# Kernel optimization log

Hardware: AMD Instinct MI355X
Metric: run time of the kernel (lower is better)

Reference implementation:

```python
import jax, jax.numpy as jnp
import numpy as np

N = 100000          # nodes
E = 6400000         # edges (avg degree 64)
V0 = 1.0            # self.v0 (source assigns v0 despite u0 arg)
W0 = 1.0            # self.w0
EPS = 1e-12         # torch F.normalize eps


def setup_inputs() -> dict:
    key = jax.random.key(0)
    k1, k2, k3, k4 = jax.random.split(key, 4)
    return {
        "x": jax.random.normal(k1, (N, 1), dtype=jnp.float32),
        "theta": jax.random.normal(k2, (N, 1), dtype=jnp.float32),
        "edge_src": jax.random.randint(k3, (E,), 0, N, dtype=jnp.int64),
        "edge_dst": jax.random.randint(k4, (E,), 0, N, dtype=jnp.int64),
    }


def reference(x, theta, edge_src, edge_dst):
    # node velocity: v = v0 * [cos(theta), sin(theta)]  -> [N, 2]
    v = V0 * jnp.concatenate([jnp.cos(theta), jnp.sin(theta)], axis=-1)

    # per-edge message: dtheta = x[src] - theta[dst]; m = [cos, sin]  -> [E, 2]
    dtheta = x[edge_src] - theta[edge_dst]            # [E, 1]
    msg = jnp.concatenate([jnp.cos(dtheta), jnp.sin(dtheta)], axis=-1)  # [E, 2]

    # mailbox mean over incoming edges per dst node (segment mean)
    seg_sum = jax.ops.segment_sum(msg, edge_dst, num_segments=N)               # [N, 2]
    cnt = jax.ops.segment_sum(jnp.ones((E, 1), msg.dtype), edge_dst, num_segments=N)
    mean_cs = seg_sum / jnp.maximum(cnt, 1.0)

    # torque: w = w0 * normalize(mean_cs)[..., 1:2]  (L2-normalize, torch eps)
    norm = jnp.maximum(jnp.linalg.norm(mean_cs, axis=-1, keepdims=True), EPS)
    w = W0 * (mean_cs / norm)[..., 1:2]               # [N, 1]

    # updated ndata packed as [v_x, v_y, w]
    return jnp.concatenate([v, w], axis=-1)           # [N, 3]
```

## Files before the change

kernel.cpp:

```cpp
#include <hip/hip_runtime.h>
#include <math.h>


#define EPS 1e-12f
#define NPART 16
#define RNODES 6250
#define RMAX 6250
#define BLK 1024

#define NBIN 512
#define BINBLK 512
#define CAP 1024
#define OCAP 262144

static __device__ __forceinline__ unsigned long long pack_cs(float xv) {
    float sn, cs;
    __sincosf(xv, &sn, &cs);
    const int ci = __float2int_rn(cs * 32768.0f);
    const int si = __float2int_rn(sn * 32768.0f);
    return (1ull << 52)
         | ((unsigned long long)(unsigned)(si + 32768) << 26)
         | (unsigned long long)(unsigned)(ci + 32768);
}

__global__ __launch_bounds__(256) void prep_pack_kernel(
        const float* __restrict__ x,
        unsigned long long* __restrict__ pu,
        int* __restrict__ oflow_cnt, int N) {
    int i = blockIdx.x * blockDim.x + threadIdx.x;
    if (i < N) pu[i] = pack_cs(x[i]);
    else if (i == N && oflow_cnt) pu[N] = 0ull;
    if (i == 0 && oflow_cnt) *oflow_cnt = 0;
}

__global__ __launch_bounds__(BINBLK) void bin_kernel(
        const int* __restrict__ esrc,
        const int* __restrict__ edst,
        unsigned* __restrict__ records,
        int* __restrict__ counts,
        unsigned long long* __restrict__ oflow,
        int* __restrict__ oflow_cnt,
        int E, int N) {
    __shared__ int lcur[NPART];
    if (threadIdx.x < NPART) lcur[threadIdx.x] = 0;
    __syncthreads();

    const int chunk = (((E + NBIN - 1) / NBIN) + 3) & ~3;
    const int beg = blockIdx.x * chunk;
    const int end = min(beg + chunk, E);
    const int end4 = beg + (max(end - beg, 0) & ~3);
    unsigned* __restrict__ myrec =
        records + (size_t)blockIdx.x * (NPART * CAP);

    for (int i = beg + threadIdx.x * 4; i < end4; i += BINBLK * 4) {
        const int4 d4 = *(const int4*)&edst[i];
        const int4 s4 = *(const int4*)&esrc[i];
        const int dv[4] = {d4.x, d4.y, d4.z, d4.w};
        const int sv[4] = {s4.x, s4.y, s4.z, s4.w};
        #pragma unroll
        for (int j = 0; j < 4; ++j) {
            const unsigned d = (unsigned)dv[j];
            const unsigned p = d / RNODES;
            const unsigned dl = d - p * RNODES;
            const unsigned rec = ((unsigned)sv[j] << 13) | dl;
            const int slot = atomicAdd(&lcur[p], 1);
            if (slot < CAP) {
                myrec[p * CAP + slot] = rec;
            } else {
                const int g = atomicAdd(oflow_cnt, 1);
                if (g < OCAP)
                    oflow[g] = ((unsigned long long)(unsigned)sv[j] << 32) | d;
            }
        }
    }
    for (int i = end4 + threadIdx.x; i < end; i += BINBLK) {
        const unsigned d = (unsigned)edst[i];
        const unsigned p = d / RNODES;
        const unsigned dl = d - p * RNODES;
        const unsigned rec = ((unsigned)esrc[i] << 13) | dl;
        const int slot = atomicAdd(&lcur[p], 1);
        if (slot < CAP) {
            myrec[p * CAP + slot] = rec;
        } else {
            const int g = atomicAdd(oflow_cnt, 1);
            if (g < OCAP)
                oflow[g] = ((unsigned long long)(unsigned)esrc[i] << 32) | d;
        }
    }

    __syncthreads();
    if (threadIdx.x < NPART) {
        const int c = min(lcur[threadIdx.x], CAP);
        const int c4 = min((c + 3) & ~3, CAP);
        for (int k = c; k < c4; ++k)
            myrec[threadIdx.x * CAP + k] = ((unsigned)N << 13);
        counts[blockIdx.x * NPART + threadIdx.x] = c4;
    }
}

__global__ __launch_bounds__(BLK, 2) void accum_kernel(
        const unsigned long long* __restrict__ pu,
        const unsigned* __restrict__ records,
        const int* __restrict__ counts,
        const unsigned long long* __restrict__ oflow,
        const int* __restrict__ oflow_cnt,
        unsigned long long* __restrict__ partials,
        int nslice) {
    __shared__ unsigned long long lacc[RMAX];
    const int p = blockIdx.x / nslice;
    const int s = blockIdx.x % nslice;

    for (int k = threadIdx.x; k < RNODES; k += BLK) lacc[k] = 0ull;
    __syncthreads();

    const int wave = threadIdx.x >> 6;
    const int lane = threadIdx.x & 63;
    const int wstep = (BLK / 64) * nslice;
    for (int c = s + wave * nslice; c < NBIN; c += wstep) {
        const int cnt = counts[c * NPART + p];
        const unsigned* __restrict__ base =
            records + ((size_t)(c * NPART + p)) * CAP;
        for (int i = lane * 4; i < cnt; i += 64 * 4) {
            const uint4 r = *(const uint4*)&base[i];
            const unsigned long long v0 = pu[r.x >> 13];
            const unsigned long long v1 = pu[r.y >> 13];
            const unsigned long long v2 = pu[r.z >> 13];
            const unsigned long long v3 = pu[r.w >> 13];
            atomicAdd(&lacc[r.x & 8191], v0);
            atomicAdd(&lacc[r.y & 8191], v1);
            atomicAdd(&lacc[r.z & 8191], v2);
            atomicAdd(&lacc[r.w & 8191], v3);
        }
    }

    if (s == 0) {
        const int oc = min(*oflow_cnt, (int)OCAP);
        const unsigned pBeg = (unsigned)(p * RNODES);
        for (int i = threadIdx.x; i < oc; i += BLK) {
            const unsigned long long e = oflow[i];
            const unsigned dl = (unsigned)e - pBeg;
            if (dl < (unsigned)RNODES) atomicAdd(&lacc[dl], pu[e >> 32]);
        }
    }

    __syncthreads();
    unsigned long long* dst = partials + (size_t)blockIdx.x * RNODES;
    for (int k = threadIdx.x; k < RNODES; k += BLK) dst[k] = lacc[k];
}

__global__ __launch_bounds__(BLK, 2) void scatter_kernel(
        const unsigned long long* __restrict__ pu,
        const int* __restrict__ esrc,
        const int* __restrict__ edst,
        unsigned long long* __restrict__ partials,
        int E, int R, int nslice) {
    __shared__ unsigned long long lacc[RMAX];
    const int p = blockIdx.x / nslice;
    const int s = blockIdx.x % nslice;
    const int pBeg = p * R;

    for (int k = threadIdx.x; k < R; k += BLK) lacc[k] = 0ull;
    __syncthreads();

    const int per = (((E + nslice - 1) / nslice) + 7) & ~7;
    const int beg = s * per;
    const int end = min(beg + per, E);
    const int end8 = beg + (max(end - beg, 0) & ~7);

    for (int i = beg + threadIdx.x * 8; i < end8; i += BLK * 8) {
        const int4 da = *(const int4*)&edst[i];
        const int4 db = *(const int4*)&edst[i + 4];
        const int4 sa = *(const int4*)&esrc[i];
        const int4 sb = *(const int4*)&esrc[i + 4];
        const unsigned dl0 = (unsigned)(da.x - pBeg);
        const unsigned dl1 = (unsigned)(da.y - pBeg);
        const unsigned dl2 = (unsigned)(da.z - pBeg);
        const unsigned dl3 = (unsigned)(da.w - pBeg);
        const unsigned dl4 = (unsigned)(db.x - pBeg);
        const unsigned dl5 = (unsigned)(db.y - pBeg);
        const unsigned dl6 = (unsigned)(db.z - pBeg);
        const unsigned dl7 = (unsigned)(db.w - pBeg);
        const bool h0 = dl0 < (unsigned)R, h1 = dl1 < (unsigned)R;
        const bool h2 = dl2 < (unsigned)R, h3 = dl3 < (unsigned)R;
        const bool h4 = dl4 < (unsigned)R, h5 = dl5 < (unsigned)R;
        const bool h6 = dl6 < (unsigned)R, h7 = dl7 < (unsigned)R;
        unsigned long long v0 = 0, v1 = 0, v2 = 0, v3 = 0;
        unsigned long long v4 = 0, v5 = 0, v6 = 0, v7 = 0;
        if (h0) v0 = pu[sa.x];
        if (h1) v1 = pu[sa.y];
        if (h2) v2 = pu[sa.z];
        if (h3) v3 = pu[sa.w];
        if (h4) v4 = pu[sb.x];
        if (h5) v5 = pu[sb.y];
        if (h6) v6 = pu[sb.z];
        if (h7) v7 = pu[sb.w];
        if (h0) atomicAdd(&lacc[dl0], v0);
        if (h1) atomicAdd(&lacc[dl1], v1);
        if (h2) atomicAdd(&lacc[dl2], v2);
        if (h3) atomicAdd(&lacc[dl3], v3);
        if (h4) atomicAdd(&lacc[dl4], v4);
        if (h5) atomicAdd(&lacc[dl5], v5);
        if (h6) atomicAdd(&lacc[dl6], v6);
        if (h7) atomicAdd(&lacc[dl7], v7);
    }
    for (int i = end8 + threadIdx.x; i < end; i += BLK) {
        const unsigned dl = (unsigned)(edst[i] - pBeg);
        if (dl < (unsigned)R) atomicAdd(&lacc[dl], pu[esrc[i]]);
    }

    __syncthreads();
    unsigned long long* dst = partials + (size_t)blockIdx.x * R;
    for (int k = threadIdx.x; k < R; k += BLK) dst[k] = lacc[k];
}

__global__ __launch_bounds__(256) void reduce_kernel(
        const float* __restrict__ theta,
        const unsigned long long* __restrict__ partials,
        float* __restrict__ out, int N, int R, int nslice) {
    const int n = blockIdx.x * blockDim.x + threadIdx.x;
    if (n >= N) return;
    const int p = n / R;
    const int j = n - p * R;
    const unsigned long long* base = partials + (size_t)p * nslice * R + j;
    unsigned long long t = 0ull;
    #pragma unroll 8
    for (int s = 0; s < nslice; ++s) t += base[(size_t)s * R];
    const long long k  = (long long)(t >> 52);
    const long long cf = (long long)(t & 0x3FFFFFFull);
    const long long sf = (long long)((t >> 26) & 0x3FFFFFFull);
    const float C  = (float)(cf - k * 32768) * (1.0f / 32768.0f);
    const float Sv = (float)(sf - k * 32768) * (1.0f / 32768.0f);
    float sn, cs;
    __sincosf(theta[n], &sn, &cs);
    const float nrm = fmaxf(sqrtf(C * C + Sv * Sv), EPS);
    out[3 * n + 0] = cs;
    out[3 * n + 1] = sn;
    out[3 * n + 2] = (cs * Sv - sn * C) / nrm;
}

__global__ __launch_bounds__(256) void prep_acc_kernel(float2* __restrict__ acc, int N) {
    int i = blockIdx.x * blockDim.x + threadIdx.x;
    if (i < N) acc[i] = make_float2(0.0f, 0.0f);
}

__global__ __launch_bounds__(256) void edge_scatter_sincos_kernel(
        const int* __restrict__ esrc,
        const int* __restrict__ edst,
        const float* __restrict__ x,
        float2* __restrict__ acc, int E) {
    const int i = (blockIdx.x * 256 + threadIdx.x) * 4;
    float* accf = (float*)acc;
    for (int k = i; k < min(i + 4, E); ++k) {
        float sn, cs;
        __sincosf(x[esrc[k]], &sn, &cs);
        const int d = edst[k];
        unsafeAtomicAdd(&accf[2 * d],     cs);
        unsafeAtomicAdd(&accf[2 * d + 1], sn);
    }
}

__global__ __launch_bounds__(256) void node_kernel(
        const float* __restrict__ theta,
        const float2* __restrict__ acc,
        float* __restrict__ out, int N) {
    int n = blockIdx.x * blockDim.x + threadIdx.x;
    if (n >= N) return;
    float sn, cs;
    __sincosf(theta[n], &sn, &cs);
    const float2 a = acc[n];
    const float nrm = fmaxf(sqrtf(a.x * a.x + a.y * a.y), EPS);
    out[3 * n + 0] = cs;
    out[3 * n + 1] = sn;
    out[3 * n + 2] = (cs * a.y - sn * a.x) / nrm;
}

extern "C" void kernel_launch(void* const* d_in, const int* in_sizes, int n_in,
                              void* d_out, int out_size, void* d_ws, size_t ws_size,
                              hipStream_t stream) {
    const float* x     = (const float*)d_in[0];
    const float* theta = (const float*)d_in[1];
    const int*   esrc  = (const int*)d_in[2];
    const int*   edst  = (const int*)d_in[3];
    float*       out   = (float*)d_out;

    const int N = in_sizes[0];
    const int E = in_sizes[2];

    if (N <= NPART * RNODES) {
        const int nslice = 32;
        const size_t part_bytes = (size_t)NPART * nslice * RNODES * 8ull;
        const size_t pu_bytes   = (((size_t)(N + 1) * 8ull) + 15) & ~(size_t)15;
        const size_t rec_bytes  = (size_t)NBIN * NPART * CAP * 4ull;
        const size_t cnt_bytes  = (size_t)NBIN * NPART * 4ull;
        const size_t ofc_bytes  = 64;
        const size_t ofl_bytes  = (size_t)OCAP * 8ull;
        const size_t total = part_bytes + pu_bytes + rec_bytes + cnt_bytes
                           + ofc_bytes + ofl_bytes;
        if (ws_size >= total) {
            char* w = (char*)d_ws;
            unsigned long long* partials = (unsigned long long*)w; w += part_bytes;
            unsigned long long* pu       = (unsigned long long*)w; w += pu_bytes;
            unsigned*           records  = (unsigned*)w;           w += rec_bytes;
            int*                counts   = (int*)w;                w += cnt_bytes;
            int*                oflow_cnt= (int*)w;                w += ofc_bytes;
            unsigned long long* oflow    = (unsigned long long*)w;

            prep_pack_kernel<<<(N + 256) / 256, 256, 0, stream>>>(
                x, pu, oflow_cnt, N);
            bin_kernel<<<NBIN, BINBLK, 0, stream>>>(
                esrc, edst, records, counts, oflow, oflow_cnt, E, N);
            accum_kernel<<<NPART * nslice, BLK, 0, stream>>>(
                pu, records, counts, oflow, oflow_cnt, partials, nslice);
            reduce_kernel<<<(N + 255) / 256, 256, 0, stream>>>(
                theta, partials, out, N, RNODES, nslice);
            return;
        }
    }

    {
        const int R = (N + NPART - 1) / NPART;
        const size_t pu_bytes = (size_t)N * sizeof(unsigned long long);
        if (R <= RMAX) {
            for (int nslice : {32, 16, 8}) {
                const size_t part_bytes =
                    (size_t)NPART * nslice * R * sizeof(unsigned long long);
                if (ws_size >= part_bytes + pu_bytes) {
                    unsigned long long* partials = (unsigned long long*)d_ws;
                    unsigned long long* pu =
                        (unsigned long long*)((char*)d_ws + part_bytes);
                    prep_pack_kernel<<<(N + 255) / 256, 256, 0, stream>>>(
                        x, pu, nullptr, N);
                    scatter_kernel<<<NPART * nslice, BLK, 0, stream>>>(
                        pu, esrc, edst, partials, E, R, nslice);
                    reduce_kernel<<<(N + 255) / 256, 256, 0, stream>>>(
                        theta, partials, out, N, R, nslice);
                    return;
                }
            }
        }
    }

    float2* acc = (float2*)d_ws;
    prep_acc_kernel<<<(N + 255) / 256, 256, 0, stream>>>(acc, N);
    edge_scatter_sincos_kernel<<<(E + 1023) / 1024, 256, 0, stream>>>(esrc, edst, x, acc, E);
    node_kernel<<<(N + 255) / 256, 256, 0, stream>>>(theta, acc, out, N);
}
```

Baseline: 149.9 us.

## Stage binned records in LDS, fuse pack into bin kernel, unroll accum by 8

The bin kernel now buffers per-partition records in shared memory one tile at a time and flushes them to global memory in contiguous wave-wide copies, instead of issuing scattered single-word stores. The cos/sin packing of x moves into the bin kernel, and a memset replaces the separate prep launch for the overflow counter. NBIN is doubled and CAP halved, and the accumulate loop processes 8 records per lane to expose more memory parallelism. In exchange, each tile adds two block barriers, and the smaller per-bin capacity may send more edges down the overflow path.

```diff
diff --git a/kernel.cpp b/kernel.cpp
--- a/kernel.cpp
+++ b/kernel.cpp
@@ -8,9 +8,11 @@
 #define RMAX 6250
 #define BLK 1024
 
-#define NBIN 512
+#define NBIN 1024
 #define BINBLK 512
-#define CAP 1024
+#define CAP 512
+#define TILE 2048
+#define BUF 256
 #define OCAP 262144
 
 static __device__ __forceinline__ unsigned long long pack_cs(float xv) {
@@ -25,76 +27,98 @@
 
 __global__ __launch_bounds__(256) void prep_pack_kernel(
         const float* __restrict__ x,
-        unsigned long long* __restrict__ pu,
-        int* __restrict__ oflow_cnt, int N) {
+        unsigned long long* __restrict__ pu, int N) {
     int i = blockIdx.x * blockDim.x + threadIdx.x;
     if (i < N) pu[i] = pack_cs(x[i]);
-    else if (i == N && oflow_cnt) pu[N] = 0ull;
-    if (i == 0 && oflow_cnt) *oflow_cnt = 0;
-}
-
-__global__ __launch_bounds__(BINBLK) void bin_kernel(
+}
+
+__global__ __launch_bounds__(BINBLK, 8) void bin_kernel(
+        const float* __restrict__ x,
         const int* __restrict__ esrc,
         const int* __restrict__ edst,
+        unsigned long long* __restrict__ pu,
         unsigned* __restrict__ records,
         int* __restrict__ counts,
         unsigned long long* __restrict__ oflow,
         int* __restrict__ oflow_cnt,
         int E, int N) {
-    __shared__ int lcur[NPART];
-    if (threadIdx.x < NPART) lcur[threadIdx.x] = 0;
+    __shared__ unsigned stage[NPART * BUF];
+    __shared__ int scur[NPART];
+    __shared__ int gcur[NPART];
+
+    {
+        const int PPB = (N + NBIN) / NBIN;
+        const int idx = blockIdx.x * PPB + threadIdx.x;
+        if (threadIdx.x < PPB && idx <= N)
+            pu[idx] = (idx < N) ? pack_cs(x[idx]) : 0ull;
+    }
+    if (threadIdx.x < NPART) { scur[threadIdx.x] = 0; gcur[threadIdx.x] = 0; }
     __syncthreads();
 
     const int chunk = (((E + NBIN - 1) / NBIN) + 3) & ~3;
     const int beg = blockIdx.x * chunk;
     const int end = min(beg + chunk, E);
-    const int end4 = beg + (max(end - beg, 0) & ~3);
     unsigned* __restrict__ myrec =
         records + (size_t)blockIdx.x * (NPART * CAP);
-
-    for (int i = beg + threadIdx.x * 4; i < end4; i += BINBLK * 4) {
-        const int4 d4 = *(const int4*)&edst[i];
-        const int4 s4 = *(const int4*)&esrc[i];
-        const int dv[4] = {d4.x, d4.y, d4.z, d4.w};
-        const int sv[4] = {s4.x, s4.y, s4.z, s4.w};
+    const int wave = threadIdx.x >> 6;
+    const int lane = threadIdx.x & 63;
+
+#define BIN_ONE(dd, ss) do {                                              \
+        const unsigned d_ = (unsigned)(dd);                               \
+        const unsigned p_ = d_ / RNODES;         \
+        const unsigned dl_ = d_ - p_ * RNODES;         \
+        const unsigned rec_ = ((unsigned)(ss) << 13) | dl_;               \
+        const int slot_ = atomicAdd(&scur[p_], 1);                        \
+        if (slot_ < BUF) {                                                \
+            stage[p_ * BUF + slot_] = rec_;                               \
+        } else {                                                          \
+            const int pos_ = gcur[p_] + slot_;      \
+            if (pos_ < CAP) myrec[p_ * CAP + pos_] = rec_;                \
+            else {                                                        \
+                const int g_ = atomicAdd(oflow_cnt, 1);                   \
+                if (g_ < OCAP)                                            \
+                    oflow[g_] = ((unsigned long long)(unsigned)(ss) << 32)\
+                              | d_;                                       \
+            }                                                             \
+        }                                                                 \
+    } while (0)
+
+    for (int tbeg = beg; tbeg < end; tbeg += TILE) {
+        const int i = tbeg + threadIdx.x * 4;
+        if (i + 4 <= end) {
+            const int4 d4 = *(const int4*)&edst[i];
+            const int4 s4 = *(const int4*)&esrc[i];
+            BIN_ONE(d4.x, s4.x);
+            BIN_ONE(d4.y, s4.y);
+            BIN_ONE(d4.z, s4.z);
+            BIN_ONE(d4.w, s4.w);
+        } else {
+            for (int k = i; k < end; ++k) BIN_ONE(edst[k], esrc[k]);
+        }
+        __syncthreads();
         #pragma unroll
-        for (int j = 0; j < 4; ++j) {
-            const unsigned d = (unsigned)dv[j];
-            const unsigned p = d / RNODES;
-            const unsigned dl = d - p * RNODES;
-            const unsigned rec = ((unsigned)sv[j] << 13) | dl;
-            const int slot = atomicAdd(&lcur[p], 1);
-            if (slot < CAP) {
-                myrec[p * CAP + slot] = rec;
-            } else {
-                const int g = atomicAdd(oflow_cnt, 1);
-                if (g < OCAP)
-                    oflow[g] = ((unsigned long long)(unsigned)sv[j] << 32) | d;
+        for (int q = 0; q < 2; ++q) {
+            const int p = wave * 2 + q;
+            const int sc = scur[p];
+            const int gc = gcur[p];
+            const int cpy = min(min(sc, (int)BUF), max((int)CAP - gc, 0));
+            for (int k = lane; k < cpy; k += 64)
+                myrec[p * CAP + gc + k] = stage[p * BUF + k];
+            if (lane == 0) {
+                gcur[p] = min(gc + sc, (int)CAP);
+                scur[p] = 0;
             }
         }
-    }
-    for (int i = end4 + threadIdx.x; i < end; i += BINBLK) {
-        const unsigned d = (unsigned)edst[i];
-        const unsigned p = d / RNODES;
-        const unsigned dl = d - p * RNODES;
-        const unsigned rec = ((unsigned)esrc[i] << 13) | dl;
-        const int slot = atomicAdd(&lcur[p], 1);
-        if (slot < CAP) {
-            myrec[p * CAP + slot] = rec;
-        } else {
-            const int g = atomicAdd(oflow_cnt, 1);
-            if (g < OCAP)
-                oflow[g] = ((unsigned long long)(unsigned)esrc[i] << 32) | d;
-        }
-    }
-
-    __syncthreads();
+        __syncthreads();
+    }
+#undef BIN_ONE
+
     if (threadIdx.x < NPART) {
-        const int c = min(lcur[threadIdx.x], CAP);
-        const int c4 = min((c + 3) & ~3, CAP);
-        for (int k = c; k < c4; ++k)
+        const int c = min(gcur[threadIdx.x], (int)CAP);
+        const int c8 = min((c + 7) & ~7, (int)CAP);
+        for (int k = c; k < c8; ++k)
             myrec[threadIdx.x * CAP + k] = ((unsigned)N << 13);
-        counts[blockIdx.x * NPART + threadIdx.x] = c4;
+        counts[blockIdx.x * NPART + threadIdx.x] = c8;
     }
 }
 
@@ -120,16 +144,25 @@
         const int cnt = counts[c * NPART + p];
         const unsigned* __restrict__ base =
             records + ((size_t)(c * NPART + p)) * CAP;
-        for (int i = lane * 4; i < cnt; i += 64 * 4) {
-            const uint4 r = *(const uint4*)&base[i];
-            const unsigned long long v0 = pu[r.x >> 13];
-            const unsigned long long v1 = pu[r.y >> 13];
-            const unsigned long long v2 = pu[r.z >> 13];
-            const unsigned long long v3 = pu[r.w >> 13];
-            atomicAdd(&lacc[r.x & 8191], v0);
-            atomicAdd(&lacc[r.y & 8191], v1);
-            atomicAdd(&lacc[r.z & 8191], v2);
-            atomicAdd(&lacc[r.w & 8191], v3);
+        for (int i = lane * 8; i < cnt; i += 64 * 8) {
+            const uint4 ra = *(const uint4*)&base[i];
+            const uint4 rb = *(const uint4*)&base[i + 4];
+            const unsigned long long v0 = pu[ra.x >> 13];
+            const unsigned long long v1 = pu[ra.y >> 13];
+            const unsigned long long v2 = pu[ra.z >> 13];
+            const unsigned long long v3 = pu[ra.w >> 13];
+            const unsigned long long v4 = pu[rb.x >> 13];
+            const unsigned long long v5 = pu[rb.y >> 13];
+            const unsigned long long v6 = pu[rb.z >> 13];
+            const unsigned long long v7 = pu[rb.w >> 13];
+            atomicAdd(&lacc[ra.x & 8191], v0);
+            atomicAdd(&lacc[ra.y & 8191], v1);
+            atomicAdd(&lacc[ra.z & 8191], v2);
+            atomicAdd(&lacc[ra.w & 8191], v3);
+            atomicAdd(&lacc[rb.x & 8191], v4);
+            atomicAdd(&lacc[rb.y & 8191], v5);
+            atomicAdd(&lacc[rb.z & 8191], v6);
+            atomicAdd(&lacc[rb.w & 8191], v7);
         }
     }
 
@@ -286,7 +319,7 @@
     const int N = in_sizes[0];
     const int E = in_sizes[2];
 
-    if (N <= NPART * RNODES) {
+    if (N <= NPART * RNODES && (size_t)(N + 1) <= (size_t)NBIN * BINBLK) {
         const int nslice = 32;
         const size_t part_bytes = (size_t)NPART * nslice * RNODES * 8ull;
         const size_t pu_bytes   = (((size_t)(N + 1) * 8ull) + 15) & ~(size_t)15;
@@ -305,10 +338,9 @@
             int*                oflow_cnt= (int*)w;                w += ofc_bytes;
             unsigned long long* oflow    = (unsigned long long*)w;
 
-            prep_pack_kernel<<<(N + 256) / 256, 256, 0, stream>>>(
-                x, pu, oflow_cnt, N);
+            hipMemsetAsync(oflow_cnt, 0, sizeof(int), stream);
             bin_kernel<<<NBIN, BINBLK, 0, stream>>>(
-                esrc, edst, records, counts, oflow, oflow_cnt, E, N);
+                x, esrc, edst, pu, records, counts, oflow, oflow_cnt, E, N);
             accum_kernel<<<NPART * nslice, BLK, 0, stream>>>(
                 pu, records, counts, oflow, oflow_cnt, partials, nslice);
             reduce_kernel<<<(N + 255) / 256, 256, 0, stream>>>(
@@ -329,7 +361,7 @@
                     unsigned long long* pu =
                         (unsigned long long*)((char*)d_ws + part_bytes);
                     prep_pack_kernel<<<(N + 255) / 256, 256, 0, stream>>>(
-                        x, pu, nullptr, N);
+                        x, pu, N);
                     scatter_kernel<<<NPART * nslice, BLK, 0, stream>>>(
                         pu, esrc, edst, partials, E, R, nslice);
                     reduce_kernel<<<(N + 255) / 256, 256, 0, stream>>>(
```

New measurement: 139.2 us. 7.1% less time.
